# Kernel tuning notes

Measured on AMD Instinct MI355X. Metric: run time of the kernel, lower is better.

## Reference

```python
import jax, jax.numpy as jnp
import numpy as np

D_MODEL = 1024
N_HEADS = 16
HEAD_DIM = D_MODEL // N_HEADS


def setup_inputs() -> dict:
    key = jax.random.key(0)
    k1, k2, k3 = jax.random.split(key, 3)
    x = jax.random.normal(k1, (4, 2048, D_MODEL), dtype=jnp.float32)
    # nn.Linear(d_model, 3*d_model, bias=False): weight [3*d_model, d_model]
    w_qkv = jax.random.normal(k2, (3 * D_MODEL, D_MODEL), dtype=jnp.float32) / np.sqrt(D_MODEL)
    w_out = jax.random.normal(k3, (D_MODEL, D_MODEL), dtype=jnp.float32) / np.sqrt(D_MODEL)
    return {"x": x, "w_qkv": w_qkv, "w_out": w_out}


def reference(x, w_qkv, w_out):
    B, T, C = x.shape
    qkv = jnp.einsum('btc,fc->btf', x, w_qkv)  # [B,T,3C]
    q, k, v = jnp.split(qkv, 3, axis=-1)

    def heads(t):
        return t.reshape(B, T, N_HEADS, HEAD_DIM).transpose(0, 2, 1, 3)  # [B,H,T,D]

    q, k, v = heads(q), heads(k), heads(v)
    scale = 1.0 / np.sqrt(HEAD_DIM).astype(np.float32)
    attn = jnp.einsum('bhqd,bhkd->bhqk', q, k) * scale  # [B,H,T,T]
    causal = jnp.tril(jnp.ones((T, T), dtype=bool))
    attn = jnp.where(causal[None, None], attn, -jnp.inf)
    attn = jax.nn.softmax(attn, axis=-1)
    out = jnp.einsum('bhqk,bhkd->bhqd', attn, v)
    out = out.transpose(0, 2, 1, 3).reshape(B, T, C)
    return jnp.einsum('btc,fc->btf', out, w_out)
```

## Files before the change

### kernel.cpp

```cpp
#include <hip/hip_runtime.h>
#include <hip/hip_bf16.h>
#include <type_traits>


typedef __attribute__((ext_vector_type(8))) short bf16x8;
typedef __attribute__((ext_vector_type(4))) float f32x4;

#define LDS_AS(p) ((__attribute__((address_space(3))) void*)(p))
#define GLB_AS(p) ((const __attribute__((address_space(1))) void*)(p))

__global__ __launch_bounds__(256) void cvt3_f32_bf16(const float* __restrict__ a,
                                                     const float* __restrict__ b,
                                                     const float* __restrict__ c,
                                                     __hip_bfloat16* __restrict__ oa,
                                                     __hip_bfloat16* __restrict__ ob,
                                                     __hip_bfloat16* __restrict__ oc,
                                                     int na4, int nb4, int nc4) {
  const int ntot = na4 + nb4 + nc4;
  for (int i = blockIdx.x * 256 + threadIdx.x; i < ntot; i += gridDim.x * 256) {
    int j = i;
    const float* in; __hip_bfloat16* out;
    if (j < na4) { in = a; out = oa; }
    else if (j < na4 + nb4) { in = b; out = ob; j -= na4; }
    else { in = c; out = oc; j -= na4 + nb4; }
    float4 v = reinterpret_cast<const float4*>(in)[j];
    __hip_bfloat16 b0 = __float2bfloat16(v.x);
    __hip_bfloat16 b1 = __float2bfloat16(v.y);
    __hip_bfloat16 b2 = __float2bfloat16(v.z);
    __hip_bfloat16 b3 = __float2bfloat16(v.w);
    ushort4 u;
    u.x = *reinterpret_cast<unsigned short*>(&b0);
    u.y = *reinterpret_cast<unsigned short*>(&b1);
    u.z = *reinterpret_cast<unsigned short*>(&b2);
    u.w = *reinterpret_cast<unsigned short*>(&b3);
    reinterpret_cast<ushort4*>(out)[j] = u;
  }
}

__global__ __launch_bounds__(512, 1) void gemm_bt256(const __hip_bfloat16* __restrict__ A,
                                                     const __hip_bfloat16* __restrict__ B,
                                                     __hip_bfloat16* __restrict__ C,
                                                     int M, int N, int K) {
  __shared__ __hip_bfloat16 As[2][256 * 64];
  __shared__ __hip_bfloat16 Bs[2][256 * 64];
  const int tid = threadIdx.x;
  const int lane = tid & 63;
  const int wid = tid >> 6;
  const int l15 = lane & 15, l4 = lane >> 4;
  const int wr = wid >> 2;
  const int wc = wid & 3;
  const int m0 = blockIdx.x * 256, n0 = blockIdx.y * 256;
  const int NT = K >> 6;
  f32x4 acc[8][4] = {};

#define STAGE256(buf, kt)                                                            \
  do {                                                                               \
    _Pragma("unroll")                                                                \
    for (int i_ = 0; i_ < 4; ++i_) {                                                 \
      const int slot_ = i_ * 512 + tid;                                              \
      const int row_ = slot_ >> 3, c8_ = slot_ & 7;                                  \
      const int gc_ = (c8_ ^ (row_ & 7)) * 8;                                        \
      __builtin_amdgcn_global_load_lds(                                              \
          GLB_AS(A + (size_t)(m0 + row_) * K + (kt) + gc_),                          \
          LDS_AS((char*)As[buf] + slot_ * 16), 16, 0, 0);                            \
      __builtin_amdgcn_global_load_lds(                                              \
          GLB_AS(B + (size_t)(n0 + row_) * K + (kt) + gc_),                          \
          LDS_AS((char*)Bs[buf] + slot_ * 16), 16, 0, 0);                            \
    }                                                                                \
  } while (0)

  STAGE256(0, 0);
  if (NT > 1) STAGE256(1, 64);

  for (int t = 0; t < NT; ++t) {
    const int cur = t & 1;
    if (t < NT - 1) asm volatile("s_waitcnt vmcnt(8)" ::: "memory");
    else            asm volatile("s_waitcnt vmcnt(0)" ::: "memory");
    __builtin_amdgcn_s_barrier();
    asm volatile("" ::: "memory");

#pragma unroll
    for (int q = 0; q < 4; ++q) {
      const int mbase = wr * 128 + (q & 1) * 64;
      const int nbase = wc * 64 + (q >> 1) * 32;
      bf16x8 af[4][2], bfr[2][2];
#pragma unroll
      for (int mi = 0; mi < 4; ++mi)
#pragma unroll
        for (int kk = 0; kk < 2; ++kk) {
          const int r = mbase + mi * 16 + l15;
          af[mi][kk] = *reinterpret_cast<const bf16x8*>(
              &As[cur][r * 64 + (((kk * 4 + l4) ^ (r & 7)) * 8)]);
        }
#pragma unroll
      for (int nj = 0; nj < 2; ++nj)
#pragma unroll
        for (int kk = 0; kk < 2; ++kk) {
          const int r = nbase + nj * 16 + l15;
          bfr[nj][kk] = *reinterpret_cast<const bf16x8*>(
              &Bs[cur][r * 64 + (((kk * 4 + l4) ^ (r & 7)) * 8)]);
        }
      __builtin_amdgcn_s_setprio(1);
#pragma unroll
      for (int mi = 0; mi < 4; ++mi)
#pragma unroll
        for (int nj = 0; nj < 2; ++nj) {
          acc[(q & 1) * 4 + mi][(q >> 1) * 2 + nj] = __builtin_amdgcn_mfma_f32_16x16x32_bf16(
              af[mi][0], bfr[nj][0], acc[(q & 1) * 4 + mi][(q >> 1) * 2 + nj], 0, 0, 0);
          acc[(q & 1) * 4 + mi][(q >> 1) * 2 + nj] = __builtin_amdgcn_mfma_f32_16x16x32_bf16(
              af[mi][1], bfr[nj][1], acc[(q & 1) * 4 + mi][(q >> 1) * 2 + nj], 0, 0, 0);
        }
      __builtin_amdgcn_s_setprio(0);
    }
    asm volatile("" ::: "memory");
    __builtin_amdgcn_s_barrier();
    asm volatile("" ::: "memory");
    if (t + 2 < NT) STAGE256(cur, (t + 2) << 6);
  }
#undef STAGE256

#pragma unroll
  for (int mi = 0; mi < 8; ++mi)
#pragma unroll
    for (int ni = 0; ni < 4; ++ni)
#pragma unroll
      for (int j = 0; j < 4; ++j) {
        const int m = m0 + wr * 128 + mi * 16 + l4 * 4 + j;
        const int n = n0 + wc * 64 + ni * 16 + l15;
        C[(size_t)m * N + n] = __float2bfloat16(acc[mi][ni][j]);
      }
}

__global__ __launch_bounds__(512, 1) void gemm_bt256x128f(const __hip_bfloat16* __restrict__ A,
                                                          const __hip_bfloat16* __restrict__ B,
                                                          float* __restrict__ C,
                                                          int M, int N, int K) {
  __shared__ __hip_bfloat16 As[2][256 * 64];
  __shared__ __hip_bfloat16 Bs[2][128 * 64];
  const int tid = threadIdx.x;
  const int lane = tid & 63;
  const int wid = tid >> 6;
  const int l15 = lane & 15, l4 = lane >> 4;
  const int wr = (wid >> 1) * 64;
  const int wc = (wid & 1) * 64;
  const int m0 = blockIdx.x * 256, n0 = blockIdx.y * 128;
  const int NT = K >> 6;
  f32x4 acc[4][4] = {};

#define STAGE2(buf, kt)                                                              \
  do {                                                                               \
    _Pragma("unroll")                                                                \
    for (int i_ = 0; i_ < 4; ++i_) {                                                 \
      const int slot_ = i_ * 512 + tid;                                              \
      const int row_ = slot_ >> 3, c8_ = slot_ & 7;                                  \
      const int gc_ = (c8_ ^ (row_ & 7)) * 8;                                        \
      __builtin_amdgcn_global_load_lds(                                              \
          GLB_AS(A + (size_t)(m0 + row_) * K + (kt) + gc_),                          \
          LDS_AS((char*)As[buf] + slot_ * 16), 16, 0, 0);                            \
    }                                                                                \
    _Pragma("unroll")                                                                \
    for (int i_ = 0; i_ < 2; ++i_) {                                                 \
      const int slot_ = i_ * 512 + tid;                                              \
      const int row_ = slot_ >> 3, c8_ = slot_ & 7;                                  \
      const int gc_ = (c8_ ^ (row_ & 7)) * 8;                                        \
      __builtin_amdgcn_global_load_lds(                                              \
          GLB_AS(B + (size_t)(n0 + row_) * K + (kt) + gc_),                          \
          LDS_AS((char*)Bs[buf] + slot_ * 16), 16, 0, 0);                            \
    }                                                                                \
  } while (0)

  STAGE2(0, 0);
  if (NT > 1) STAGE2(1, 64);

  for (int t = 0; t < NT; ++t) {
    const int cur = t & 1;
    if (t < NT - 1) asm volatile("s_waitcnt vmcnt(6)" ::: "memory");
    else            asm volatile("s_waitcnt vmcnt(0)" ::: "memory");
    __builtin_amdgcn_s_barrier();
    asm volatile("" ::: "memory");

#pragma unroll
    for (int kk = 0; kk < 2; ++kk) {
      bf16x8 af[4], bfr[4];
#pragma unroll
      for (int mi = 0; mi < 4; ++mi) {
        const int r = wr + mi * 16 + l15;
        af[mi] = *reinterpret_cast<const bf16x8*>(
            &As[cur][r * 64 + (((kk * 4 + l4) ^ (r & 7)) * 8)]);
      }
#pragma unroll
      for (int ni = 0; ni < 4; ++ni) {
        const int r = wc + ni * 16 + l15;
        bfr[ni] = *reinterpret_cast<const bf16x8*>(
            &Bs[cur][r * 64 + (((kk * 4 + l4) ^ (r & 7)) * 8)]);
      }
      __builtin_amdgcn_s_setprio(1);
#pragma unroll
      for (int mi = 0; mi < 4; ++mi)
#pragma unroll
        for (int ni = 0; ni < 4; ++ni)
          acc[mi][ni] = __builtin_amdgcn_mfma_f32_16x16x32_bf16(af[mi], bfr[ni], acc[mi][ni], 0, 0, 0);
      __builtin_amdgcn_s_setprio(0);
    }
    asm volatile("" ::: "memory");
    __builtin_amdgcn_s_barrier();
    asm volatile("" ::: "memory");
    if (t + 2 < NT) STAGE2(cur, (t + 2) << 6);
  }
#undef STAGE2

#pragma unroll
  for (int mi = 0; mi < 4; ++mi)
#pragma unroll
    for (int ni = 0; ni < 4; ++ni)
#pragma unroll
      for (int j = 0; j < 4; ++j) {
        const int m = m0 + wr + mi * 16 + l4 * 4 + j;
        const int n = n0 + wc + ni * 16 + l15;
        C[(size_t)m * N + n] = acc[mi][ni][j];
      }
}

__global__ __launch_bounds__(512, 2) void attn_causal(const __hip_bfloat16* __restrict__ qkv,
                                                      __hip_bfloat16* __restrict__ o) {
  constexpr int T = 2048, F = 3072, C = 1024;
  __shared__ __hip_bfloat16 Ks[2][64 * 72];
  __shared__ __hip_bfloat16 Vts[2][64 * 72];
  __shared__ __hip_bfloat16 Ps[8][16 * 72];
  const int tid = threadIdx.x;
  const int wid = tid >> 6, lane = tid & 63;
  const int l15 = lane & 15, l4 = lane >> 4;
  const int x = blockIdx.x, h = blockIdx.y, b = blockIdx.z;
  const int qt = (wid < 4) ? x : (7 - x);
  const int nt = 4 * (7 - x) + 4;
  const int tmax = 4 * qt + (wid & 3);
  const int hoff = h * 64;
  const __hip_bfloat16* base = qkv + (size_t)b * T * F;
  const int Q0 = qt * 256 + (wid & 3) * 64;

  constexpr float SC = 0.125f * 1.44269504088896f;

  bf16x8 aq[4][2];
#pragma unroll
  for (int f = 0; f < 4; ++f)
#pragma unroll
    for (int kk = 0; kk < 2; ++kk) {
      bf16x8 q = *reinterpret_cast<const bf16x8*>(base + (size_t)(Q0 + f * 16 + l15) * F + hoff + kk * 32 + l4 * 8);
#pragma unroll
      for (int e = 0; e < 8; ++e) {
        const unsigned short raw = (unsigned short)q[e];
        const float fv = __uint_as_float((unsigned)raw << 16) * SC;
        __hip_bfloat16 qs = __float2bfloat16(fv);
        q[e] = *reinterpret_cast<short*>(&qs);
      }
      aq[f][kk] = q;
    }

  f32x4 acc[4][4] = {};
  float mrun[4], lrun[4];
#pragma unroll
  for (int f = 0; f < 4; ++f) { mrun[f] = -1e30f; lrun[f] = 0.f; }

  const int sV = tid;
  const int sK = tid - 256;
  bf16x8 sreg0, sreg1;
  if (wid < 4) {
    const size_t vr = (size_t)(2 * (sV >> 3)) * F + hoff + 2 * C + (sV & 7) * 8;
    sreg0 = *reinterpret_cast<const bf16x8*>(base + vr);
    sreg1 = *reinterpret_cast<const bf16x8*>(base + vr + F);
  } else {
    sreg0 = *reinterpret_cast<const bf16x8*>(base + (size_t)(sK >> 3) * F + hoff + C + (sK & 7) * 8);
    sreg1 = *reinterpret_cast<const bf16x8*>(base + (size_t)(32 + (sK >> 3)) * F + hoff + C + (sK & 7) * 8);
  }

  for (int t = 0; t < nt; ++t) {
    const int cur = t & 1;
    if (wid < 4) {
      const unsigned short* a0 = reinterpret_cast<const unsigned short*>(&sreg0);
      const unsigned short* a1 = reinterpret_cast<const unsigned short*>(&sreg1);
      const int c8 = sV & 7, r2 = sV >> 3;
      unsigned pk[8], tw[8], pkr[8];
#pragma unroll
      for (int j = 0; j < 8; ++j) pk[j] = (unsigned)a0[j] | ((unsigned)a1[j] << 16);
#pragma unroll
      for (int j = 0; j < 8; ++j) tw[j] = (c8 & 4) ? pk[(j + 4) & 7] : pk[j];
#pragma unroll
      for (int j = 0; j < 8; ++j) pkr[j] = (c8 & 2) ? tw[(j + 2) & 7] : tw[j];
#pragma unroll
      for (int j = 0; j < 8; ++j) tw[j] = (c8 & 1) ? pkr[(j + 1) & 7] : pkr[j];
#pragma unroll
      for (int jj = 0; jj < 8; ++jj) {
        const int d = c8 * 8 + ((jj + c8) & 7);
        *reinterpret_cast<unsigned*>(&Vts[cur][d * 72 + 2 * r2]) = tw[jj];
      }
    } else {
      *reinterpret_cast<bf16x8*>(&Ks[cur][(sK >> 3) * 72 + (sK & 7) * 8]) = sreg0;
      *reinterpret_cast<bf16x8*>(&Ks[cur][(32 + (sK >> 3)) * 72 + (sK & 7) * 8]) = sreg1;
    }
    __syncthreads();
    if (t + 1 < nt) {
      const int kn = (t + 1) * 64;
      if (wid < 4) {
        const size_t vr = (size_t)(kn + 2 * (sV >> 3)) * F + hoff + 2 * C + (sV & 7) * 8;
        sreg0 = *reinterpret_cast<const bf16x8*>(base + vr);
        sreg1 = *reinterpret_cast<const bf16x8*>(base + vr + F);
      } else {
        sreg0 = *reinterpret_cast<const bf16x8*>(base + (size_t)(kn + (sK >> 3)) * F + hoff + C + (sK & 7) * 8);
        sreg1 = *reinterpret_cast<const bf16x8*>(base + (size_t)(kn + 32 + (sK >> 3)) * F + hoff + C + (sK & 7) * 8);
      }
    }
    if (t > tmax) continue;
    const bool diag = (t == tmax);

    bf16x8 kf[4][2], vf[4][2];
#pragma unroll
    for (int kt = 0; kt < 4; ++kt)
#pragma unroll
      for (int kk = 0; kk < 2; ++kk)
        kf[kt][kk] = *reinterpret_cast<const bf16x8*>(&Ks[cur][(kt * 16 + l15) * 72 + kk * 32 + l4 * 8]);
#pragma unroll
    for (int di = 0; di < 4; ++di)
#pragma unroll
      for (int kk = 0; kk < 2; ++kk)
        vf[di][kk] = *reinterpret_cast<const bf16x8*>(&Vts[cur][(di * 16 + l15) * 72 + kk * 32 + l4 * 8]);

    __hip_bfloat16* pw = Ps[wid];
#pragma unroll
    for (int f = 0; f < 4; ++f) {
      f32x4 s[4];
#pragma unroll
      for (int kt = 0; kt < 4; ++kt) {
        f32x4 z = {};
        z = __builtin_amdgcn_mfma_f32_16x16x32_bf16(kf[kt][0], aq[f][0], z, 0, 0, 0);
        z = __builtin_amdgcn_mfma_f32_16x16x32_bf16(kf[kt][1], aq[f][1], z, 0, 0, 0);
        s[kt] = z;
      }
      if (diag) {
        const int ql = f * 16 + l15;
#pragma unroll
        for (int kt = 0; kt < 4; ++kt)
#pragma unroll
          for (int j = 0; j < 4; ++j) {
            const int kvl = kt * 16 + l4 * 4 + j;
            s[kt][j] = (kvl <= ql) ? s[kt][j] : -1e30f;
          }
      }

      float t0 = fmaxf(fmaxf(s[0][0], s[0][1]), s[0][2]);
      float t1 = fmaxf(fmaxf(s[0][3], s[1][0]), s[1][1]);
      float t2 = fmaxf(fmaxf(s[1][2], s[1][3]), s[2][0]);
      float t3 = fmaxf(fmaxf(s[2][1], s[2][2]), s[2][3]);
      float t4 = fmaxf(fmaxf(s[3][0], s[3][1]), s[3][2]);
      float mt = fmaxf(fmaxf(fmaxf(t0, t1), fmaxf(t2, t3)), fmaxf(t4, s[3][3]));
      mt = fmaxf(mt, __shfl_xor(mt, 16, 64));
      mt = fmaxf(mt, __shfl_xor(mt, 32, 64));
      const bool defer = __all(mt <= mrun[f] + 8.f);
      const float mnew = defer ? mrun[f] : fmaxf(mrun[f], mt);
      float rs = 0.f;
#pragma unroll
      for (int kt = 0; kt < 4; ++kt) {
        float p0 = exp2f(s[kt][0] - mnew), p1 = exp2f(s[kt][1] - mnew);
        float p2 = exp2f(s[kt][2] - mnew), p3 = exp2f(s[kt][3] - mnew);
        s[kt][0] = p0; s[kt][1] = p1; s[kt][2] = p2; s[kt][3] = p3;
        rs += (p0 + p1) + (p2 + p3);
      }
      rs += __shfl_xor(rs, 16, 64);
      rs += __shfl_xor(rs, 32, 64);
      if (defer) {
        lrun[f] += rs;
      } else {
        const float sco = exp2f(mrun[f] - mnew);
        lrun[f] = lrun[f] * sco + rs;
        mrun[f] = mnew;
#pragma unroll
        for (int di = 0; di < 4; ++di) acc[f][di] *= sco;
      }

#pragma unroll
      for (int kt = 0; kt < 4; ++kt) {
        unsigned w0, w1;
        asm("v_cvt_pk_bf16_f32 %0, %1, %2" : "=v"(w0) : "v"(s[kt][0]), "v"(s[kt][1]));
        asm("v_cvt_pk_bf16_f32 %0, %1, %2" : "=v"(w1) : "v"(s[kt][2]), "v"(s[kt][3]));
        unsigned long long dw = (unsigned long long)w0 | ((unsigned long long)w1 << 32);
        *reinterpret_cast<unsigned long long*>(&pw[l15 * 72 + kt * 16 + l4 * 4]) = dw;
      }
      asm volatile("s_waitcnt lgkmcnt(0)" ::: "memory");
      bf16x8 pa0 = *reinterpret_cast<const bf16x8*>(pw + l15 * 72 + l4 * 8);
      bf16x8 pa1 = *reinterpret_cast<const bf16x8*>(pw + l15 * 72 + 32 + l4 * 8);

#pragma unroll
      for (int di = 0; di < 4; ++di) {
        acc[f][di] = __builtin_amdgcn_mfma_f32_16x16x32_bf16(vf[di][0], pa0, acc[f][di], 0, 0, 0);
        acc[f][di] = __builtin_amdgcn_mfma_f32_16x16x32_bf16(vf[di][1], pa1, acc[f][di], 0, 0, 0);
      }
    }
  }

#pragma unroll
  for (int f = 0; f < 4; ++f) {
    const float inv = 1.0f / lrun[f];
    __hip_bfloat16* op = o + (size_t)((size_t)b * T + Q0 + f * 16 + l15) * C + hoff;
#pragma unroll
    for (int di = 0; di < 4; ++di) {
      ushort4 u;
      __hip_bfloat16 e0 = __float2bfloat16(acc[f][di][0] * inv);
      __hip_bfloat16 e1 = __float2bfloat16(acc[f][di][1] * inv);
      __hip_bfloat16 e2 = __float2bfloat16(acc[f][di][2] * inv);
      __hip_bfloat16 e3 = __float2bfloat16(acc[f][di][3] * inv);
      u.x = *reinterpret_cast<unsigned short*>(&e0);
      u.y = *reinterpret_cast<unsigned short*>(&e1);
      u.z = *reinterpret_cast<unsigned short*>(&e2);
      u.w = *reinterpret_cast<unsigned short*>(&e3);
      *reinterpret_cast<ushort4*>(op + di * 16 + l4 * 4) = u;
    }
  }
}

extern "C" void kernel_launch(void* const* d_in, const int* in_sizes, int n_in,
                              void* d_out, int out_size, void* d_ws, size_t ws_size,
                              hipStream_t stream) {
  const float* x = (const float*)d_in[0];
  const float* w_qkv = (const float*)d_in[1];
  const float* w_out = (const float*)d_in[2];
  float* out = (float*)d_out;

  constexpr int B = 4, T = 2048, C = 1024, F = 3 * C;
  constexpr int M = B * T;

  __hip_bfloat16* xb = (__hip_bfloat16*)d_ws;
  __hip_bfloat16* wqkvb = xb + (size_t)M * C;
  __hip_bfloat16* woutb = wqkvb + (size_t)F * C;
  __hip_bfloat16* qkvb = woutb + (size_t)C * C;
  __hip_bfloat16* attnb = qkvb + (size_t)M * F;

  constexpr int na4 = M * C / 4, nb4 = F * C / 4, nc4 = C * C / 4;
  cvt3_f32_bf16<<<2048, 256, 0, stream>>>(x, w_qkv, w_out, xb, wqkvb, woutb, na4, nb4, nc4);

  gemm_bt256<<<dim3(M / 256, F / 256), 512, 0, stream>>>(xb, wqkvb, qkvb, M, F, C);

  attn_causal<<<dim3(4, 16, B), 512, 0, stream>>>(qkvb, attnb);

  gemm_bt256x128f<<<dim3(M / 256, C / 128), 512, 0, stream>>>(attnb, woutb, out, M, C, C);
}
```

Before: 219.6 us.

## Switch attention to 32x32x16 MFMA and pass P through registers

Rewrites the causal attention inner loop to use 32x32x16 bf16 MFMA tiles instead of 16x16x32. The softmax probabilities are rearranged into the B-operand layout with cross-half lane shuffles, so the per-wave LDS round trip for P is gone. Launch bounds drop to one block per SIMD occupancy hint, giving more registers for the larger accumulators. This removes LDS write/read plus waitcnt stalls and halves the number of MFMA issues, but may lower occupancy.

```diff
diff --git a/kernel.cpp b/kernel.cpp
--- a/kernel.cpp
+++ b/kernel.cpp
@@ -5,6 +5,8 @@
 
 typedef __attribute__((ext_vector_type(8))) short bf16x8;
 typedef __attribute__((ext_vector_type(4))) float f32x4;
+typedef __attribute__((ext_vector_type(16))) float f32x16;
+typedef __attribute__((ext_vector_type(4))) int i32x4;
 
 #define LDS_AS(p) ((__attribute__((address_space(3))) void*)(p))
 #define GLB_AS(p) ((const __attribute__((address_space(1))) void*)(p))
@@ -221,15 +223,14 @@
       }
 }
 
-__global__ __launch_bounds__(512, 2) void attn_causal(const __hip_bfloat16* __restrict__ qkv,
+__global__ __launch_bounds__(512, 1) void attn_causal(const __hip_bfloat16* __restrict__ qkv,
                                                       __hip_bfloat16* __restrict__ o) {
   constexpr int T = 2048, F = 3072, C = 1024;
   __shared__ __hip_bfloat16 Ks[2][64 * 72];
   __shared__ __hip_bfloat16 Vts[2][64 * 72];
-  __shared__ __hip_bfloat16 Ps[8][16 * 72];
   const int tid = threadIdx.x;
   const int wid = tid >> 6, lane = tid & 63;
-  const int l15 = lane & 15, l4 = lane >> 4;
+  const int l31 = lane & 31, lh = lane >> 5;
   const int x = blockIdx.x, h = blockIdx.y, b = blockIdx.z;
   const int qt = (wid < 4) ? x : (7 - x);
   const int nt = 4 * (7 - x) + 4;
@@ -240,12 +241,13 @@
 
   constexpr float SC = 0.125f * 1.44269504088896f;
 
-  bf16x8 aq[4][2];
-#pragma unroll
-  for (int f = 0; f < 4; ++f)
-#pragma unroll
-    for (int kk = 0; kk < 2; ++kk) {
-      bf16x8 q = *reinterpret_cast<const bf16x8*>(base + (size_t)(Q0 + f * 16 + l15) * F + hoff + kk * 32 + l4 * 8);
+  bf16x8 aq[2][4];
+#pragma unroll
+  for (int c = 0; c < 2; ++c)
+#pragma unroll
+    for (int s = 0; s < 4; ++s) {
+      bf16x8 q = *reinterpret_cast<const bf16x8*>(
+          base + (size_t)(Q0 + c * 32 + l31) * F + hoff + s * 16 + lh * 8);
 #pragma unroll
       for (int e = 0; e < 8; ++e) {
         const unsigned short raw = (unsigned short)q[e];
@@ -253,13 +255,13 @@
         __hip_bfloat16 qs = __float2bfloat16(fv);
         q[e] = *reinterpret_cast<short*>(&qs);
       }
-      aq[f][kk] = q;
-    }
-
-  f32x4 acc[4][4] = {};
-  float mrun[4], lrun[4];
-#pragma unroll
-  for (int f = 0; f < 4; ++f) { mrun[f] = -1e30f; lrun[f] = 0.f; }
+      aq[c][s] = q;
+    }
+
+  f32x16 acc[2][2] = {};
+  float mrun[2], lrun[2];
+#pragma unroll
+  for (int c = 0; c < 2; ++c) { mrun[c] = -1e30f; lrun[c] = 0.f; }
 
   const int sV = tid;
   const int sK = tid - 256;
@@ -312,107 +314,111 @@
     if (t > tmax) continue;
     const bool diag = (t == tmax);
 
-    bf16x8 kf[4][2], vf[4][2];
-#pragma unroll
-    for (int kt = 0; kt < 4; ++kt)
-#pragma unroll
-      for (int kk = 0; kk < 2; ++kk)
-        kf[kt][kk] = *reinterpret_cast<const bf16x8*>(&Ks[cur][(kt * 16 + l15) * 72 + kk * 32 + l4 * 8]);
-#pragma unroll
-    for (int di = 0; di < 4; ++di)
-#pragma unroll
-      for (int kk = 0; kk < 2; ++kk)
-        vf[di][kk] = *reinterpret_cast<const bf16x8*>(&Vts[cur][(di * 16 + l15) * 72 + kk * 32 + l4 * 8]);
-
-    __hip_bfloat16* pw = Ps[wid];
-#pragma unroll
-    for (int f = 0; f < 4; ++f) {
-      f32x4 s[4];
-#pragma unroll
-      for (int kt = 0; kt < 4; ++kt) {
-        f32x4 z = {};
-        z = __builtin_amdgcn_mfma_f32_16x16x32_bf16(kf[kt][0], aq[f][0], z, 0, 0, 0);
-        z = __builtin_amdgcn_mfma_f32_16x16x32_bf16(kf[kt][1], aq[f][1], z, 0, 0, 0);
-        s[kt] = z;
-      }
+    bf16x8 ka[2][4], va[2][4];
+#pragma unroll
+    for (int hh = 0; hh < 2; ++hh)
+#pragma unroll
+      for (int s = 0; s < 4; ++s)
+        ka[hh][s] = *reinterpret_cast<const bf16x8*>(
+            &Ks[cur][(hh * 32 + l31) * 72 + s * 16 + lh * 8]);
+#pragma unroll
+    for (int dh = 0; dh < 2; ++dh)
+#pragma unroll
+      for (int s = 0; s < 4; ++s)
+        va[dh][s] = *reinterpret_cast<const bf16x8*>(
+            &Vts[cur][(dh * 32 + l31) * 72 + s * 16 + lh * 8]);
+
+#pragma unroll
+    for (int c = 0; c < 2; ++c) {
+      f32x16 sh0 = {}, sh1 = {};
+#pragma unroll
+      for (int s = 0; s < 4; ++s)
+        sh0 = __builtin_amdgcn_mfma_f32_32x32x16_bf16(ka[0][s], aq[c][s], sh0, 0, 0, 0);
+#pragma unroll
+      for (int s = 0; s < 4; ++s)
+        sh1 = __builtin_amdgcn_mfma_f32_32x32x16_bf16(ka[1][s], aq[c][s], sh1, 0, 0, 0);
+
       if (diag) {
-        const int ql = f * 16 + l15;
-#pragma unroll
-        for (int kt = 0; kt < 4; ++kt)
-#pragma unroll
-          for (int j = 0; j < 4; ++j) {
-            const int kvl = kt * 16 + l4 * 4 + j;
-            s[kt][j] = (kvl <= ql) ? s[kt][j] : -1e30f;
-          }
-      }
-
-      float t0 = fmaxf(fmaxf(s[0][0], s[0][1]), s[0][2]);
-      float t1 = fmaxf(fmaxf(s[0][3], s[1][0]), s[1][1]);
-      float t2 = fmaxf(fmaxf(s[1][2], s[1][3]), s[2][0]);
-      float t3 = fmaxf(fmaxf(s[2][1], s[2][2]), s[2][3]);
-      float t4 = fmaxf(fmaxf(s[3][0], s[3][1]), s[3][2]);
-      float mt = fmaxf(fmaxf(fmaxf(t0, t1), fmaxf(t2, t3)), fmaxf(t4, s[3][3]));
-      mt = fmaxf(mt, __shfl_xor(mt, 16, 64));
+        const int ql = c * 32 + l31;
+#pragma unroll
+        for (int r = 0; r < 16; ++r) {
+          const int kvl = (r & 3) + 8 * (r >> 2) + 4 * lh;
+          sh0[r] = (kvl <= ql) ? sh0[r] : -1e30f;
+          sh1[r] = (kvl + 32 <= ql) ? sh1[r] : -1e30f;
+        }
+      }
+
+      float mt = -1e30f;
+#pragma unroll
+      for (int r = 0; r < 16; ++r) mt = fmaxf(mt, fmaxf(sh0[r], sh1[r]));
       mt = fmaxf(mt, __shfl_xor(mt, 32, 64));
-      const bool defer = __all(mt <= mrun[f] + 8.f);
-      const float mnew = defer ? mrun[f] : fmaxf(mrun[f], mt);
+      const bool defer = __all(mt <= mrun[c] + 8.f);
+      const float mnew = defer ? mrun[c] : fmaxf(mrun[c], mt);
       float rs = 0.f;
 #pragma unroll
-      for (int kt = 0; kt < 4; ++kt) {
-        float p0 = exp2f(s[kt][0] - mnew), p1 = exp2f(s[kt][1] - mnew);
-        float p2 = exp2f(s[kt][2] - mnew), p3 = exp2f(s[kt][3] - mnew);
-        s[kt][0] = p0; s[kt][1] = p1; s[kt][2] = p2; s[kt][3] = p3;
-        rs += (p0 + p1) + (p2 + p3);
-      }
-      rs += __shfl_xor(rs, 16, 64);
+      for (int r = 0; r < 16; ++r) {
+        const float p0 = exp2f(sh0[r] - mnew), p1 = exp2f(sh1[r] - mnew);
+        sh0[r] = p0; sh1[r] = p1;
+        rs += p0 + p1;
+      }
       rs += __shfl_xor(rs, 32, 64);
       if (defer) {
-        lrun[f] += rs;
+        lrun[c] += rs;
       } else {
-        const float sco = exp2f(mrun[f] - mnew);
-        lrun[f] = lrun[f] * sco + rs;
-        mrun[f] = mnew;
-#pragma unroll
-        for (int di = 0; di < 4; ++di) acc[f][di] *= sco;
-      }
-
-#pragma unroll
-      for (int kt = 0; kt < 4; ++kt) {
+        const float sco = exp2f(mrun[c] - mnew);
+        lrun[c] = lrun[c] * sco + rs;
+        mrun[c] = mnew;
+        acc[c][0] *= sco;
+        acc[c][1] *= sco;
+      }
+
+#pragma unroll
+      for (int s = 0; s < 4; ++s) {
+        const int r0 = (s & 1) * 8;
+        unsigned pkX0, pkX1, pkY0, pkY1;
+        if (s < 2) {
+          asm("v_cvt_pk_bf16_f32 %0, %1, %2" : "=v"(pkX0) : "v"(sh0[r0 + 0]), "v"(sh0[r0 + 1]));
+          asm("v_cvt_pk_bf16_f32 %0, %1, %2" : "=v"(pkX1) : "v"(sh0[r0 + 2]), "v"(sh0[r0 + 3]));
+          asm("v_cvt_pk_bf16_f32 %0, %1, %2" : "=v"(pkY0) : "v"(sh0[r0 + 4]), "v"(sh0[r0 + 5]));
+          asm("v_cvt_pk_bf16_f32 %0, %1, %2" : "=v"(pkY1) : "v"(sh0[r0 + 6]), "v"(sh0[r0 + 7]));
+        } else {
+          asm("v_cvt_pk_bf16_f32 %0, %1, %2" : "=v"(pkX0) : "v"(sh1[r0 + 0]), "v"(sh1[r0 + 1]));
+          asm("v_cvt_pk_bf16_f32 %0, %1, %2" : "=v"(pkX1) : "v"(sh1[r0 + 2]), "v"(sh1[r0 + 3]));
+          asm("v_cvt_pk_bf16_f32 %0, %1, %2" : "=v"(pkY0) : "v"(sh1[r0 + 4]), "v"(sh1[r0 + 5]));
+          asm("v_cvt_pk_bf16_f32 %0, %1, %2" : "=v"(pkY1) : "v"(sh1[r0 + 6]), "v"(sh1[r0 + 7]));
+        }
+        const int send0 = (int)(lh ? pkX0 : pkY0);
+        const int send1 = (int)(lh ? pkX1 : pkY1);
+        const unsigned recv0 = (unsigned)__shfl_xor(send0, 32, 64);
+        const unsigned recv1 = (unsigned)__shfl_xor(send1, 32, 64);
+        i32x4 pw;
+        pw[0] = (int)(lh ? recv0 : pkX0);
+        pw[1] = (int)(lh ? recv1 : pkX1);
+        pw[2] = (int)(lh ? pkY0 : recv0);
+        pw[3] = (int)(lh ? pkY1 : recv1);
+        bf16x8 pb = *reinterpret_cast<bf16x8*>(&pw);
+        acc[c][0] = __builtin_amdgcn_mfma_f32_32x32x16_bf16(va[0][s], pb, acc[c][0], 0, 0, 0);
+        acc[c][1] = __builtin_amdgcn_mfma_f32_32x32x16_bf16(va[1][s], pb, acc[c][1], 0, 0, 0);
+      }
+    }
+  }
+
+#pragma unroll
+  for (int c = 0; c < 2; ++c) {
+    const float inv = 1.0f / lrun[c];
+    __hip_bfloat16* op = o + (size_t)((size_t)b * T + Q0 + c * 32 + l31) * C + hoff;
+#pragma unroll
+    for (int dh = 0; dh < 2; ++dh)
+#pragma unroll
+      for (int G = 0; G < 4; ++G) {
         unsigned w0, w1;
-        asm("v_cvt_pk_bf16_f32 %0, %1, %2" : "=v"(w0) : "v"(s[kt][0]), "v"(s[kt][1]));
-        asm("v_cvt_pk_bf16_f32 %0, %1, %2" : "=v"(w1) : "v"(s[kt][2]), "v"(s[kt][3]));
-        unsigned long long dw = (unsigned long long)w0 | ((unsigned long long)w1 << 32);
-        *reinterpret_cast<unsigned long long*>(&pw[l15 * 72 + kt * 16 + l4 * 4]) = dw;
-      }
-      asm volatile("s_waitcnt lgkmcnt(0)" ::: "memory");
-      bf16x8 pa0 = *reinterpret_cast<const bf16x8*>(pw + l15 * 72 + l4 * 8);
-      bf16x8 pa1 = *reinterpret_cast<const bf16x8*>(pw + l15 * 72 + 32 + l4 * 8);
-
-#pragma unroll
-      for (int di = 0; di < 4; ++di) {
-        acc[f][di] = __builtin_amdgcn_mfma_f32_16x16x32_bf16(vf[di][0], pa0, acc[f][di], 0, 0, 0);
-        acc[f][di] = __builtin_amdgcn_mfma_f32_16x16x32_bf16(vf[di][1], pa1, acc[f][di], 0, 0, 0);
-      }
-    }
-  }
-
-#pragma unroll
-  for (int f = 0; f < 4; ++f) {
-    const float inv = 1.0f / lrun[f];
-    __hip_bfloat16* op = o + (size_t)((size_t)b * T + Q0 + f * 16 + l15) * C + hoff;
-#pragma unroll
-    for (int di = 0; di < 4; ++di) {
-      ushort4 u;
-      __hip_bfloat16 e0 = __float2bfloat16(acc[f][di][0] * inv);
-      __hip_bfloat16 e1 = __float2bfloat16(acc[f][di][1] * inv);
-      __hip_bfloat16 e2 = __float2bfloat16(acc[f][di][2] * inv);
-      __hip_bfloat16 e3 = __float2bfloat16(acc[f][di][3] * inv);
-      u.x = *reinterpret_cast<unsigned short*>(&e0);
-      u.y = *reinterpret_cast<unsigned short*>(&e1);
-      u.z = *reinterpret_cast<unsigned short*>(&e2);
-      u.w = *reinterpret_cast<unsigned short*>(&e3);
-      *reinterpret_cast<ushort4*>(op + di * 16 + l4 * 4) = u;
-    }
+        const float e0 = acc[c][dh][4 * G + 0] * inv, e1 = acc[c][dh][4 * G + 1] * inv;
+        const float e2 = acc[c][dh][4 * G + 2] * inv, e3 = acc[c][dh][4 * G + 3] * inv;
+        asm("v_cvt_pk_bf16_f32 %0, %1, %2" : "=v"(w0) : "v"(e0), "v"(e1));
+        asm("v_cvt_pk_bf16_f32 %0, %1, %2" : "=v"(w1) : "v"(e2), "v"(e3));
+        const unsigned long long dw = (unsigned long long)w0 | ((unsigned long long)w1 << 32);
+        *reinterpret_cast<unsigned long long*>(op + dh * 32 + G * 8 + 4 * lh) = dw;
+      }
   }
 }
 
```

Result: slower. 256.0 us (+16.6%).
